# Kernel optimization log

Hardware: AMD Instinct MI355X
Metric: run time of the kernel (lower is better)

## Reference

```python
import jax, jax.numpy as jnp
import numpy as np

N_NODES = 10000
N_EDGES = 640000
HIDDEN = 128
N_LAYERS = 3
DECAY_RATE = 1.0


def setup_inputs() -> dict:
    key = jax.random.key(0)
    ks = jax.random.split(key, 16)
    D, L = HIDDEN, N_LAYERS
    s = 1.0 / np.sqrt(D)
    inp = {
        "x": jax.random.normal(ks[0], (N_NODES, D), dtype=jnp.float32),
        "edge_index": jax.random.randint(ks[1], (2, N_EDGES), 0, N_NODES, dtype=jnp.int32),
        "confidences": jax.random.uniform(ks[2], (N_NODES,), dtype=jnp.float32),
        # per-layer message MLP params, stacked over layers: [L, D, D] / [L, D]
        "msg_W1": jax.random.normal(ks[3], (L, D, D), dtype=jnp.float32) * s,
        "msg_b1": jnp.zeros((L, D), dtype=jnp.float32),
        "msg_W2": jax.random.normal(ks[4], (L, D, D), dtype=jnp.float32) * s,
        "msg_b2": jnp.zeros((L, D), dtype=jnp.float32),
        # per-layer self MLP params
        "self_W1": jax.random.normal(ks[5], (L, D, D), dtype=jnp.float32) * s,
        "self_b1": jnp.zeros((L, D), dtype=jnp.float32),
        "self_W2": jax.random.normal(ks[6], (L, D, D), dtype=jnp.float32) * s,
        "self_b2": jnp.zeros((L, D), dtype=jnp.float32),
        # layer-importance score net: Linear(D,D) -> ReLU -> Linear(D,1)
        "score_W1": jax.random.normal(ks[7], (D, D), dtype=jnp.float32) * s,
        "score_b1": jnp.zeros((D,), dtype=jnp.float32),
        "score_W2": jax.random.normal(ks[8], (D, 1), dtype=jnp.float32) * s,
        "score_b2": jnp.zeros((1,), dtype=jnp.float32),
    }
    return inp


def _mlp2(h, W1, b1, W2, b2):
    return jax.nn.relu(h @ W1 + b1) @ W2 + b2


def reference(x, edge_index, confidences,
              msg_W1, msg_b1, msg_W2, msg_b2,
              self_W1, self_b1, self_W2, self_b2,
              score_W1, score_b1, score_W2, score_b2):
    src, dst = edge_index[0], edge_index[1]
    # confidence-weighted edge weights: exp(-decay * |c_src - c_dst|)
    edge_weights = jnp.exp(-DECAY_RATE * jnp.abs(confidences[src] - confidences[dst]))  # [E]

    h = x
    layer_outputs = []
    for i in range(N_LAYERS):
        messages = _mlp2(h[src], msg_W1[i], msg_b1[i], msg_W2[i], msg_b2[i])  # [E, D]
        messages = messages * edge_weights[:, None]
        aggr = jax.ops.segment_sum(messages, dst, num_segments=N_NODES)  # [N, D]
        self_loop = _mlp2(h, self_W1[i], self_b1[i], self_W2[i], self_b2[i])
        h = jax.nn.relu(aggr + self_loop)  # dropout is identity in eval mode
        layer_outputs.append(h)

    stacked = jnp.stack(layer_outputs, axis=0)  # [L, N, D]
    scores = _mlp2(stacked, score_W1, score_b1, score_W2, score_b2)[..., 0]  # [L, N]
    layer_weights = jax.nn.softmax(scores, axis=0)  # softmax over layers
    output = jnp.sum(layer_weights[:, :, None] * stacked, axis=0)  # [N, D]
    return output, stacked, layer_weights
```

## Files before the change

kernel.cpp:

```cpp
#include <hip/hip_runtime.h>

#define NN 10000
#define NE 640000
#define D 128
#define NF (NN * D)
#define WS 136
#define WBYTES (D * WS * 2)
#define WCHUNKS (WBYTES / 1024)
#define NBLK 100
#define EPB (NE / NBLK)

typedef __bf16 bf16x8 __attribute__((ext_vector_type(8)));
typedef __bf16 bf16x2 __attribute__((ext_vector_type(2)));
typedef float f32x4 __attribute__((ext_vector_type(4)));

__device__ __forceinline__ void async_copy16(const void* g, void* l) {
    __builtin_amdgcn_global_load_lds(
        (const __attribute__((address_space(1))) unsigned int*)g,
        (__attribute__((address_space(3))) unsigned int*)l, 16, 0, 0);
}


__global__ __launch_bounds__(256) void hist_lds_kernel(const int* __restrict__ ei,
                                                       int* __restrict__ cnt_blk,
                                                       int* __restrict__ local_rank) {
    __shared__ int hist[NN];
    int b = blockIdx.x, t = threadIdx.x;
    for (int i = t; i < NN; i += 256) hist[i] = 0;
    __syncthreads();
    int base = b * EPB;
#pragma unroll 1
    for (int i = 0; i < EPB / 256; i++) {
        int e = base + i * 256 + t;
        int d = ei[NE + e];
        local_rank[e] = atomicAdd(&hist[d], 1);
    }
    __syncthreads();
    for (int i = t; i < NN; i += 256) cnt_blk[b * NN + i] = hist[i];
}

__global__ void colsum_kernel(int* __restrict__ cnt_blk, int* __restrict__ cnt) {
    int n = blockIdx.x * 256 + threadIdx.x;
    if (n >= NN) return;
    int acc = 0;
#pragma unroll 4
    for (int b = 0; b < NBLK; b++) {
        int v = cnt_blk[b * NN + n];
        cnt_blk[b * NN + n] = acc;
        acc += v;
    }
    cnt[n] = acc;
}

__global__ void scan_kernel(const int* __restrict__ cnt, int* __restrict__ row_ptr) {
    __shared__ int lds[256];
    int t = threadIdx.x;
    const int CH = (NN + 255) / 256;
    int base = t * CH;
    int s = 0;
    for (int i = 0; i < CH; i++) {
        int idx = base + i;
        if (idx < NN) s += cnt[idx];
    }
    lds[t] = s;
    __syncthreads();
    for (int off = 1; off < 256; off <<= 1) {
        int v = (t >= off) ? lds[t - off] : 0;
        __syncthreads();
        lds[t] += v;
        __syncthreads();
    }
    int run = (t == 0) ? 0 : lds[t - 1];
    for (int i = 0; i < CH; i++) {
        int idx = base + i;
        if (idx < NN) {
            row_ptr[idx] = run;
            run += cnt[idx];
        }
    }
    if (t == 255) row_ptr[NN] = lds[255];
}

__global__ void scatter_kernel(const int* __restrict__ ei, const float* __restrict__ conf,
                               const int* __restrict__ local_rank,
                               const int* __restrict__ cnt_blk,
                               const int* __restrict__ row_ptr, float2* __restrict__ meta) {
    int e = blockIdx.x * 256 + threadIdx.x;
    if (e >= NE) return;
    int s = ei[e];
    int d = ei[NE + e];
    int blk = e / EPB;
    int pos = row_ptr[d] + cnt_blk[blk * NN + d] + local_rank[e];
    meta[pos] = make_float2(__int_as_float(s), expf(-fabsf(conf[s] - conf[d])));
}

__global__ __launch_bounds__(256) void prep_all_kernel(
    const float2* __restrict__ x2, bf16x2* __restrict__ xbf,
    const float* __restrict__ mW1, const float* __restrict__ mW2,
    const float* __restrict__ sW1, const float* __restrict__ sW2,
    const float* __restrict__ scW1, __bf16* __restrict__ wt) {
    int b = blockIdx.x;
    if (b < 2500) {
        int i = b * 256 + threadIdx.x;
        float2 v = x2[i];
        bf16x2 o;
        o.x = (__bf16)v.x;
        o.y = (__bf16)v.y;
        xbf[i] = o;
    } else {
        int m = b - 2500;
        const float* W = (m < 3)   ? mW1 + (size_t)m * D * D
                       : (m < 6)   ? mW2 + (size_t)(m - 3) * D * D
                       : (m < 9)   ? sW1 + (size_t)(m - 6) * D * D
                       : (m < 12)  ? sW2 + (size_t)(m - 9) * D * D
                                   : scW1;
        __bf16* o = wt + (size_t)m * D * WS;
        for (int i = threadIdx.x; i < D * D; i += 256) {
            int k = i >> 7, n = i & 127;
            o[n * WS + k] = (__bf16)W[i];
        }
    }
}


__global__ __launch_bounds__(128) void mlp_pair_mfma(
    const __bf16* __restrict__ Abf,
    const __bf16* __restrict__ Wt1a, const float* __restrict__ b1a,
    const __bf16* __restrict__ Wt2a, const float* __restrict__ b2a, __bf16* __restrict__ Mbf,
    const __bf16* __restrict__ Wt1b, const float* __restrict__ b1b,
    const __bf16* __restrict__ Wt2b, const float* __restrict__ b2b, float* __restrict__ Cself) {
    const __bf16* Wt1 = blockIdx.y ? Wt1b : Wt1a;
    const float* b1 = blockIdx.y ? b1b : b1a;
    const __bf16* Wt2 = blockIdx.y ? Wt2b : Wt2a;
    const float* b2 = blockIdx.y ? b2b : b2a;

    __shared__ __align__(16) __bf16 Wl[2][D * WS];
    __shared__ __align__(16) __bf16 Tl[2][16 * WS];
    int t = threadIdx.x;
    int wid = t >> 6, lane = t & 63;
    int m16 = lane & 15, q = lane >> 4;

    for (int c = wid; c < WCHUNKS; c += 2)
        async_copy16((const char*)Wt1 + c * 1024 + lane * 16,
                     (char*)&Wl[0][0] + c * 1024 + lane * 16);

    int row0 = blockIdx.x * 32 + wid * 16;
    int arow = min(row0 + m16, NN - 1);

    bf16x8 af[4];
#pragma unroll
    for (int kk = 0; kk < 4; kk++) af[kk] = *(const bf16x8*)&Abf[(size_t)arow * D + kk * 32 + q * 8];
    float b1v[8], b2v[8];
#pragma unroll
    for (int ct = 0; ct < 8; ct++) { b1v[ct] = b1[ct * 16 + m16]; b2v[ct] = b2[ct * 16 + m16]; }

    __syncthreads();

    for (int c = wid; c < WCHUNKS; c += 2)
        async_copy16((const char*)Wt2 + c * 1024 + lane * 16,
                     (char*)&Wl[1][0] + c * 1024 + lane * 16);

    f32x4 acc[8];
#pragma unroll
    for (int ct = 0; ct < 8; ct++) acc[ct] = (f32x4){0.f, 0.f, 0.f, 0.f};
#pragma unroll
    for (int kk = 0; kk < 4; kk++) {
#pragma unroll
        for (int ct = 0; ct < 8; ct++) {
            bf16x8 b = *(const bf16x8*)&Wl[0][(ct * 16 + m16) * WS + kk * 32 + q * 8];
            acc[ct] = __builtin_amdgcn_mfma_f32_16x16x32_bf16(af[kk], b, acc[ct], 0, 0, 0);
        }
    }
#pragma unroll
    for (int ct = 0; ct < 8; ct++) {
#pragma unroll
        for (int r = 0; r < 4; r++) {
            float v = fmaxf(acc[ct][r] + b1v[ct], 0.f);
            Tl[wid][(q * 4 + r) * WS + ct * 16 + m16] = (__bf16)v;
        }
    }
    __syncthreads();

#pragma unroll
    for (int ct = 0; ct < 8; ct++) acc[ct] = (f32x4){0.f, 0.f, 0.f, 0.f};
#pragma unroll
    for (int kk = 0; kk < 4; kk++) {
        bf16x8 a = *(const bf16x8*)&Tl[wid][m16 * WS + kk * 32 + q * 8];
#pragma unroll
        for (int ct = 0; ct < 8; ct++) {
            bf16x8 b = *(const bf16x8*)&Wl[1][(ct * 16 + m16) * WS + kk * 32 + q * 8];
            acc[ct] = __builtin_amdgcn_mfma_f32_16x16x32_bf16(a, b, acc[ct], 0, 0, 0);
        }
    }
    if (blockIdx.y == 0) {
#pragma unroll
        for (int ct = 0; ct < 8; ct++) {
#pragma unroll
            for (int r = 0; r < 4; r++) {
                int row = row0 + q * 4 + r;
                if (row < NN) Mbf[(size_t)row * D + ct * 16 + m16] = (__bf16)(acc[ct][r] + b2v[ct]);
            }
        }
    } else {
#pragma unroll
        for (int ct = 0; ct < 8; ct++) {
#pragma unroll
            for (int r = 0; r < 4; r++) {
                int row = row0 + q * 4 + r;
                if (row < NN) Cself[(size_t)row * D + ct * 16 + m16] = acc[ct][r] + b2v[ct];
            }
        }
    }
}


__global__ __launch_bounds__(256) void aggregate_kernel(
    const uint4* __restrict__ Mbf4, const float4* __restrict__ Mself4,
    const int* __restrict__ row_ptr, const float2* __restrict__ meta,
    float4* __restrict__ out4, bf16x8* __restrict__ stbf8) {
    int wid = (blockIdx.x * 256 + threadIdx.x) >> 6;
    int lane = threadIdx.x & 63;
    int q = lane >> 4, l4 = lane & 15;
    int beg = row_ptr[wid], end = row_ptr[wid + 1];
    float a[8] = {0.f, 0.f, 0.f, 0.f, 0.f, 0.f, 0.f, 0.f};
    for (int j = beg; j < end; j += 32) {
        float2 m[8];
        uint4 g[8];
#pragma unroll
        for (int u = 0; u < 8; u++) {
            int jj = j + 4 * u + q;
            m[u] = make_float2(__int_as_float(0), 0.f);
            if (jj < end) m[u] = meta[jj];
        }
#pragma unroll
        for (int u = 0; u < 8; u++) {
            g[u] = make_uint4(0u, 0u, 0u, 0u);
            if (j + 4 * u + q < end) g[u] = Mbf4[(size_t)__float_as_int(m[u].x) * 16 + l4];
        }
#pragma unroll
        for (int u = 0; u < 8; u++) {
            float w = m[u].y;
            a[0] = fmaf(w, __uint_as_float(g[u].x << 16), a[0]);
            a[1] = fmaf(w, __uint_as_float(g[u].x & 0xFFFF0000u), a[1]);
            a[2] = fmaf(w, __uint_as_float(g[u].y << 16), a[2]);
            a[3] = fmaf(w, __uint_as_float(g[u].y & 0xFFFF0000u), a[3]);
            a[4] = fmaf(w, __uint_as_float(g[u].z << 16), a[4]);
            a[5] = fmaf(w, __uint_as_float(g[u].z & 0xFFFF0000u), a[5]);
            a[6] = fmaf(w, __uint_as_float(g[u].w << 16), a[6]);
            a[7] = fmaf(w, __uint_as_float(g[u].w & 0xFFFF0000u), a[7]);
        }
    }
#pragma unroll
    for (int i = 0; i < 8; i++) {
        a[i] += __shfl_xor(a[i], 16);
        a[i] += __shfl_xor(a[i], 32);
    }
    if (q == 0) {
        float4 sv0 = Mself4[(size_t)wid * 32 + 2 * l4];
        float4 sv1 = Mself4[(size_t)wid * 32 + 2 * l4 + 1];
        float4 r0, r1;
        r0.x = fmaxf(a[0] + sv0.x, 0.f);
        r0.y = fmaxf(a[1] + sv0.y, 0.f);
        r0.z = fmaxf(a[2] + sv0.z, 0.f);
        r0.w = fmaxf(a[3] + sv0.w, 0.f);
        r1.x = fmaxf(a[4] + sv1.x, 0.f);
        r1.y = fmaxf(a[5] + sv1.y, 0.f);
        r1.z = fmaxf(a[6] + sv1.z, 0.f);
        r1.w = fmaxf(a[7] + sv1.w, 0.f);
        out4[(size_t)wid * 32 + 2 * l4] = r0;
        out4[(size_t)wid * 32 + 2 * l4 + 1] = r1;
        bf16x8 hb;
        hb[0] = (__bf16)r0.x; hb[1] = (__bf16)r0.y;
        hb[2] = (__bf16)r0.z; hb[3] = (__bf16)r0.w;
        hb[4] = (__bf16)r1.x; hb[5] = (__bf16)r1.y;
        hb[6] = (__bf16)r1.z; hb[7] = (__bf16)r1.w;
        stbf8[(size_t)wid * 16 + l4] = hb;
    }
}


__global__ __launch_bounds__(256) void score_finalize_mfma(
    const __bf16* __restrict__ stbf, const float* __restrict__ st,
    const __bf16* __restrict__ Wt1, const float* __restrict__ b1,
    const float* __restrict__ w2, const float* __restrict__ b2,
    float* __restrict__ out, float* __restrict__ lw_out) {
    __shared__ __align__(16) __bf16 Wl[D * WS];
    __shared__ float sc_l[3][64];
    __shared__ float lw_l[3][64];
    int t = threadIdx.x;
    int wid = t >> 6, lane = t & 63;
    int m16 = lane & 15, q = lane >> 4;
    int row0 = blockIdx.x * 64;

    for (int c = wid; c < WCHUNKS; c += 4)
        async_copy16((const char*)Wt1 + c * 1024 + lane * 16,
                     (char*)&Wl[0] + c * 1024 + lane * 16);
    __syncthreads();

    int arow = min(row0 + wid * 16 + m16, NN - 1);
    float bb = b2[0];

    for (int l = 0; l < 3; l++) {
        const __bf16* A = stbf + (size_t)l * NF;
        f32x4 acc[8];
#pragma unroll
        for (int ct = 0; ct < 8; ct++) acc[ct] = (f32x4){0.f, 0.f, 0.f, 0.f};
#pragma unroll
        for (int kk = 0; kk < 4; kk++) {
            bf16x8 a = *(const bf16x8*)&A[(size_t)arow * D + kk * 32 + q * 8];
#pragma unroll
            for (int ct = 0; ct < 8; ct++) {
                bf16x8 b = *(const bf16x8*)&Wl[(ct * 16 + m16) * WS + kk * 32 + q * 8];
                acc[ct] = __builtin_amdgcn_mfma_f32_16x16x32_bf16(a, b, acc[ct], 0, 0, 0);
            }
        }
        float p[4] = {0.f, 0.f, 0.f, 0.f};
#pragma unroll
        for (int ct = 0; ct < 8; ct++) {
            float bv = b1[ct * 16 + m16];
            float wv = w2[ct * 16 + m16];
#pragma unroll
            for (int r = 0; r < 4; r++) p[r] += fmaxf(acc[ct][r] + bv, 0.f) * wv;
        }
#pragma unroll
        for (int r = 0; r < 4; r++) {
#pragma unroll
            for (int off = 1; off < 16; off <<= 1) p[r] += __shfl_xor(p[r], off);
            if (m16 == 0) sc_l[l][wid * 16 + q * 4 + r] = p[r] + bb;
        }
    }
    __syncthreads();

    if (t < 64) {
        int row = row0 + t;
        float s0 = sc_l[0][t], s1 = sc_l[1][t], s2 = sc_l[2][t];
        float m = fmaxf(s0, fmaxf(s1, s2));
        float e0 = expf(s0 - m), e1 = expf(s1 - m), e2 = expf(s2 - m);
        float inv = 1.f / (e0 + e1 + e2);
        lw_l[0][t] = e0 * inv;
        lw_l[1][t] = e1 * inv;
        lw_l[2][t] = e2 * inv;
        if (row < NN) {
            lw_out[row] = e0 * inv;
            lw_out[NN + row] = e1 * inv;
            lw_out[2 * NN + row] = e2 * inv;
        }
    }
    __syncthreads();

    for (int i = t; i < 64 * 32; i += 256) {
        int r = i >> 5, c4 = i & 31;
        int row = row0 + r;
        if (row >= NN) break;
        float4 v0 = ((const float4*)(st + (size_t)row * D))[c4];
        float4 v1 = ((const float4*)(st + (size_t)NF + (size_t)row * D))[c4];
        float4 v2 = ((const float4*)(st + 2 * (size_t)NF + (size_t)row * D))[c4];
        float w0 = lw_l[0][r], w1 = lw_l[1][r], w2v = lw_l[2][r];
        float4 o;
        o.x = w0 * v0.x + w1 * v1.x + w2v * v2.x;
        o.y = w0 * v0.y + w1 * v1.y + w2v * v2.y;
        o.z = w0 * v0.z + w1 * v1.z + w2v * v2.z;
        o.w = w0 * v0.w + w1 * v1.w + w2v * v2.w;
        ((float4*)(out + (size_t)row * D))[c4] = o;
    }
}

extern "C" void kernel_launch(void* const* d_in, const int* in_sizes, int n_in,
                              void* d_out, int out_size, void* d_ws, size_t ws_size,
                              hipStream_t stream) {
    const float* x = (const float*)d_in[0];
    const int* ei = (const int*)d_in[1];
    const float* conf = (const float*)d_in[2];
    const float* msg_W1 = (const float*)d_in[3];
    const float* msg_b1 = (const float*)d_in[4];
    const float* msg_W2 = (const float*)d_in[5];
    const float* msg_b2 = (const float*)d_in[6];
    const float* self_W1 = (const float*)d_in[7];
    const float* self_b1 = (const float*)d_in[8];
    const float* self_W2 = (const float*)d_in[9];
    const float* self_b2 = (const float*)d_in[10];
    const float* score_W1 = (const float*)d_in[11];
    const float* score_b1 = (const float*)d_in[12];
    const float* score_W2 = (const float*)d_in[13];
    const float* score_b2 = (const float*)d_in[14];

    float* out = (float*)d_out;
    float* out_stacked = out + NF;
    float* out_lw = out + 4 * (size_t)NF;

    float* w = (float*)d_ws;
    float* Mself = w;
    float2* meta = (float2*)(w + (size_t)NF);
    __bf16* xbf = (__bf16*)(meta + NE);
    __bf16* stbf = xbf + (size_t)NF;
    __bf16* Mbf = stbf + 3 * (size_t)NF;
    __bf16* wt = Mbf + (size_t)NF;
    int* local_rank = (int*)(wt + 13 * (size_t)D * WS);
    int* cnt_blk = local_rank + NE;
    int* row_ptr = cnt_blk + NBLK * NN;
    int* cnt = row_ptr + NN + 1;

    const size_t MAT = (size_t)D * WS;
    const int GE = (NE + 255) / 256;
    const int GB32 = (NN + 31) / 32;
    const int GB64 = (NN + 63) / 64;

    hist_lds_kernel<<<NBLK, 256, 0, stream>>>(ei, cnt_blk, local_rank);
    prep_all_kernel<<<2513, 256, 0, stream>>>((const float2*)x, (bf16x2*)xbf,
                                              msg_W1, msg_W2, self_W1, self_W2, score_W1, wt);
    colsum_kernel<<<(NN + 255) / 256, 256, 0, stream>>>(cnt_blk, cnt);
    scan_kernel<<<1, 256, 0, stream>>>(cnt, row_ptr);
    scatter_kernel<<<GE, 256, 0, stream>>>(ei, conf, local_rank, cnt_blk, row_ptr, meta);

    for (int l = 0; l < 3; l++) {
        const __bf16* a_in = (l == 0) ? xbf : stbf + (size_t)(l - 1) * NF;
        mlp_pair_mfma<<<dim3(GB32, 2), 128, 0, stream>>>(
            a_in,
            wt + (size_t)l * MAT, msg_b1 + (size_t)l * D,
            wt + (size_t)(3 + l) * MAT, msg_b2 + (size_t)l * D, Mbf,
            wt + (size_t)(6 + l) * MAT, self_b1 + (size_t)l * D,
            wt + (size_t)(9 + l) * MAT, self_b2 + (size_t)l * D, Mself);
        aggregate_kernel<<<NN / 4, 256, 0, stream>>>(
            (const uint4*)Mbf, (const float4*)Mself, row_ptr, meta,
            (float4*)(out_stacked + (size_t)l * NF),
            (bf16x8*)(stbf + (size_t)l * NF));
    }

    score_finalize_mfma<<<GB64, 256, 0, stream>>>(
        stbf, out_stacked, wt + 12 * MAT, score_b1, score_W2, score_b2, out, out_lw);
}
```

Baseline: 284.9 us.

## Pad CSR rows to 32 edges, shuffle-broadcast prefetched edge metadata, fuse prep kernels

Each node's CSR segment is padded to a multiple of 32 in a zeroed metadata buffer. The aggregate loop can then drop its bounds checks, since padded entries point to node 0 with zero weight. Each wave loads one coalesced metadata entry per lane, prefetches the next chunk, and broadcasts source ids and weights via shuffles instead of redundant per-quad loads. The histogram and the bf16 conversion/weight-transpose kernels are merged into one launch. In exchange it adds a memset of the padded buffer and extra wasted gathers on padding entries.

```diff
diff --git a/kernel.cpp b/kernel.cpp
--- a/kernel.cpp
+++ b/kernel.cpp
@@ -9,6 +9,7 @@
 #define WCHUNKS (WBYTES / 1024)
 #define NBLK 100
 #define EPB (NE / NBLK)
+#define MPAD 1000000
 
 typedef __bf16 bf16x8 __attribute__((ext_vector_type(8)));
 typedef __bf16 bf16x2 __attribute__((ext_vector_type(2)));
@@ -21,22 +22,45 @@
 }
 
 
-__global__ __launch_bounds__(256) void hist_lds_kernel(const int* __restrict__ ei,
-                                                       int* __restrict__ cnt_blk,
-                                                       int* __restrict__ local_rank) {
+__global__ __launch_bounds__(256) void hist_prep_kernel(
+    const int* __restrict__ ei, int* __restrict__ cnt_blk, int* __restrict__ local_rank,
+    const float2* __restrict__ x2, bf16x2* __restrict__ xbf,
+    const float* __restrict__ mW1, const float* __restrict__ mW2,
+    const float* __restrict__ sW1, const float* __restrict__ sW2,
+    const float* __restrict__ scW1, __bf16* __restrict__ wt) {
     __shared__ int hist[NN];
     int b = blockIdx.x, t = threadIdx.x;
-    for (int i = t; i < NN; i += 256) hist[i] = 0;
-    __syncthreads();
-    int base = b * EPB;
+    if (b < NBLK) {
+        for (int i = t; i < NN; i += 256) hist[i] = 0;
+        __syncthreads();
+        int base = b * EPB;
 #pragma unroll 1
-    for (int i = 0; i < EPB / 256; i++) {
-        int e = base + i * 256 + t;
-        int d = ei[NE + e];
-        local_rank[e] = atomicAdd(&hist[d], 1);
-    }
-    __syncthreads();
-    for (int i = t; i < NN; i += 256) cnt_blk[b * NN + i] = hist[i];
+        for (int i = 0; i < EPB / 256; i++) {
+            int e = base + i * 256 + t;
+            local_rank[e] = atomicAdd(&hist[ei[NE + e]], 1);
+        }
+        __syncthreads();
+        for (int i = t; i < NN; i += 256) cnt_blk[b * NN + i] = hist[i];
+    } else if (b < 2600) {
+        int i = (b - NBLK) * 256 + t;
+        float2 v = x2[i];
+        bf16x2 o;
+        o.x = (__bf16)v.x;
+        o.y = (__bf16)v.y;
+        xbf[i] = o;
+    } else {
+        int m = b - 2600;
+        const float* W = (m < 3)   ? mW1 + (size_t)m * D * D
+                       : (m < 6)   ? mW2 + (size_t)(m - 3) * D * D
+                       : (m < 9)   ? sW1 + (size_t)(m - 6) * D * D
+                       : (m < 12)  ? sW2 + (size_t)(m - 9) * D * D
+                                   : scW1;
+        __bf16* o = wt + (size_t)m * D * WS;
+        for (int i = t; i < D * D; i += 256) {
+            int k = i >> 7, n = i & 127;
+            o[n * WS + k] = (__bf16)W[i];
+        }
+    }
 }
 
 __global__ void colsum_kernel(int* __restrict__ cnt_blk, int* __restrict__ cnt) {
@@ -60,7 +84,7 @@
     int s = 0;
     for (int i = 0; i < CH; i++) {
         int idx = base + i;
-        if (idx < NN) s += cnt[idx];
+        if (idx < NN) s += (cnt[idx] + 31) & ~31;
     }
     lds[t] = s;
     __syncthreads();
@@ -75,7 +99,7 @@
         int idx = base + i;
         if (idx < NN) {
             row_ptr[idx] = run;
-            run += cnt[idx];
+            run += (cnt[idx] + 31) & ~31;
         }
     }
     if (t == 255) row_ptr[NN] = lds[255];
@@ -94,34 +118,6 @@
     meta[pos] = make_float2(__int_as_float(s), expf(-fabsf(conf[s] - conf[d])));
 }
 
-__global__ __launch_bounds__(256) void prep_all_kernel(
-    const float2* __restrict__ x2, bf16x2* __restrict__ xbf,
-    const float* __restrict__ mW1, const float* __restrict__ mW2,
-    const float* __restrict__ sW1, const float* __restrict__ sW2,
-    const float* __restrict__ scW1, __bf16* __restrict__ wt) {
-    int b = blockIdx.x;
-    if (b < 2500) {
-        int i = b * 256 + threadIdx.x;
-        float2 v = x2[i];
-        bf16x2 o;
-        o.x = (__bf16)v.x;
-        o.y = (__bf16)v.y;
-        xbf[i] = o;
-    } else {
-        int m = b - 2500;
-        const float* W = (m < 3)   ? mW1 + (size_t)m * D * D
-                       : (m < 6)   ? mW2 + (size_t)(m - 3) * D * D
-                       : (m < 9)   ? sW1 + (size_t)(m - 6) * D * D
-                       : (m < 12)  ? sW2 + (size_t)(m - 9) * D * D
-                                   : scW1;
-        __bf16* o = wt + (size_t)m * D * WS;
-        for (int i = threadIdx.x; i < D * D; i += 256) {
-            int k = i >> 7, n = i & 127;
-            o[n * WS + k] = (__bf16)W[i];
-        }
-    }
-}
-
 
 __global__ __launch_bounds__(128) void mlp_pair_mfma(
     const __bf16* __restrict__ Abf,
@@ -220,26 +216,26 @@
     float4* __restrict__ out4, bf16x8* __restrict__ stbf8) {
     int wid = (blockIdx.x * 256 + threadIdx.x) >> 6;
     int lane = threadIdx.x & 63;
-    int q = lane >> 4, l4 = lane & 15;
+    int q = lane >> 4, l4 = lane & 15, l5 = lane & 31;
     int beg = row_ptr[wid], end = row_ptr[wid + 1];
     float a[8] = {0.f, 0.f, 0.f, 0.f, 0.f, 0.f, 0.f, 0.f};
+    float2 mcur = meta[beg + l5];
     for (int j = beg; j < end; j += 32) {
-        float2 m[8];
+        float2 mnext = meta[j + 32 + l5];
+        int srcid[8];
+        float wgt[8];
+#pragma unroll
+        for (int u = 0; u < 8; u++) {
+            int sl = 4 * u + q;
+            srcid[u] = __float_as_int(__shfl(mcur.x, sl));
+            wgt[u] = __shfl(mcur.y, sl);
+        }
         uint4 g[8];
 #pragma unroll
+        for (int u = 0; u < 8; u++) g[u] = Mbf4[(size_t)srcid[u] * 16 + l4];
+#pragma unroll
         for (int u = 0; u < 8; u++) {
-            int jj = j + 4 * u + q;
-            m[u] = make_float2(__int_as_float(0), 0.f);
-            if (jj < end) m[u] = meta[jj];
-        }
-#pragma unroll
-        for (int u = 0; u < 8; u++) {
-            g[u] = make_uint4(0u, 0u, 0u, 0u);
-            if (j + 4 * u + q < end) g[u] = Mbf4[(size_t)__float_as_int(m[u].x) * 16 + l4];
-        }
-#pragma unroll
-        for (int u = 0; u < 8; u++) {
-            float w = m[u].y;
+            float w = wgt[u];
             a[0] = fmaf(w, __uint_as_float(g[u].x << 16), a[0]);
             a[1] = fmaf(w, __uint_as_float(g[u].x & 0xFFFF0000u), a[1]);
             a[2] = fmaf(w, __uint_as_float(g[u].y << 16), a[2]);
@@ -249,6 +245,7 @@
             a[6] = fmaf(w, __uint_as_float(g[u].w << 16), a[6]);
             a[7] = fmaf(w, __uint_as_float(g[u].w & 0xFFFF0000u), a[7]);
         }
+        mcur = mnext;
     }
 #pragma unroll
     for (int i = 0; i < 8; i++) {
@@ -391,7 +388,7 @@
     float* w = (float*)d_ws;
     float* Mself = w;
     float2* meta = (float2*)(w + (size_t)NF);
-    __bf16* xbf = (__bf16*)(meta + NE);
+    __bf16* xbf = (__bf16*)(meta + MPAD);
     __bf16* stbf = xbf + (size_t)NF;
     __bf16* Mbf = stbf + 3 * (size_t)NF;
     __bf16* wt = Mbf + (size_t)NF;
@@ -405,9 +402,10 @@
     const int GB32 = (NN + 31) / 32;
     const int GB64 = (NN + 63) / 64;
 
-    hist_lds_kernel<<<NBLK, 256, 0, stream>>>(ei, cnt_blk, local_rank);
-    prep_all_kernel<<<2513, 256, 0, stream>>>((const float2*)x, (bf16x2*)xbf,
-                                              msg_W1, msg_W2, self_W1, self_W2, score_W1, wt);
+    hipMemsetAsync(meta, 0, (size_t)MPAD * sizeof(float2), stream);
+    hist_prep_kernel<<<2613, 256, 0, stream>>>(ei, cnt_blk, local_rank,
+                                               (const float2*)x, (bf16x2*)xbf,
+                                               msg_W1, msg_W2, self_W1, self_W2, score_W1, wt);
     colsum_kernel<<<(NN + 255) / 256, 256, 0, stream>>>(cnt_blk, cnt);
     scan_kernel<<<1, 256, 0, stream>>>(cnt, row_ptr);
     scatter_kernel<<<GE, 256, 0, stream>>>(ei, conf, local_rank, cnt_blk, row_ptr, meta);
```

After: 254.2 us. 10.8% less time.
